# Optimization experiments

Measured on AMD Instinct MI355X. Metric: run time of the kernel, lower is better.

Reference implementation:

```python
import jax, jax.numpy as jnp
import numpy as np

K = 3        # kernel_size
UM = 2       # um_dim
EPS = 1e-6
SLOPE = 0.01 # F.leaky_relu default negative slope


def setup_inputs() -> dict:
    key = jax.random.key(0)
    k1, k2, k3 = jax.random.split(key, 3)
    B, C, H, Wd = 16, 64, 64, 64
    O = 64
    xx = jax.random.normal(k1, (B, C, H, Wd), dtype=jnp.float32)
    W = jax.random.normal(k2, (O, C, K, K), dtype=jnp.float32) * 0.05
    b = jax.random.normal(k3, (O,), dtype=jnp.float32) * 0.05
    return {"xx": xx, "W": W, "b": b}


def reference(xx, W, b):
    B, C, H, Wd = xx.shape
    O = W.shape[0]
    p = (K - 1) // 2
    # replicate pad (mode='replicate' in torch == 'edge' in numpy/jax)
    xp = jnp.pad(xx, ((0, 0), (0, 0), (p, p), (p, p)), mode='edge')
    # unfold -> patches[b, c, i, j, h, w] = xp[b, c, h+i, w+j]; stride==1
    pats = jnp.stack(
        [xp[:, :, i:i + H, j:j + Wd] for i in range(K) for j in range(K)],
        axis=2,
    ).reshape(B, C, K, K, H, Wd)
    # min-max "std" normalization over (channel-group, ki, kj)
    g = pats.reshape(B, C // UM, UM, K, K, H, Wd)
    stds = (g.max(axis=(1, 3, 4), keepdims=True)
            - g.min(axis=(1, 3, 4), keepdims=True))  # [B,1,UM,1,1,H,W]
    normed = (g / (stds + EPS)).reshape(B, C, K, K, H, Wd)
    # patch-conv with stride=k on the unfolded image is equivalent to this
    # per-position contraction; big[b,c,h*k+j, w*k+i] = normed[b,c,i,j,h,w]
    # so the kernel indexes as W[o, c, j, i].
    out = jnp.einsum('bcijhw,ocji->bohw', normed, W) + b[None, :, None, None]
    out = jnp.where(out >= 0, out, SLOPE * out)  # leaky_relu
    # inverse transform: re-scale by (stds + eps)
    stds_s = stds.reshape(B, 1, UM, H, Wd)
    out = out.reshape(B, O // UM, UM, H, Wd) * (stds_s + EPS)
    return out.reshape(B, O, H, Wd)
```

## Files before the change

### kernel.cpp

```cpp
#include <hip/hip_runtime.h>
#include <hip/hip_bf16.h>

#define B_  16
#define C_  64
#define H_  64
#define W_  64
#define O_  64
#define EPS 1e-6f
#define SLOPE 0.01f

typedef __bf16  bf16x8 __attribute__((ext_vector_type(8)));
typedef float   f32x4  __attribute__((ext_vector_type(4)));

#define WLDS_OFF 0
#define WLDS_SZ  92160
#define XT_OFF   92160
#define XT_SZ    36864
#define PMIN_OFF 129024
#define PMAX_OFF 131072
#define SINV_OFF 133120
#define SEPS_OFF 134144
#define SMEM_SZ  135168

__device__ __forceinline__ unsigned short f2bf(float f) {
  unsigned u = __float_as_uint(f);
  u += 0x7fffu + ((u >> 16) & 1u);
  return (unsigned short)(u >> 16);
}

__global__ void wtransform_kernel(const float* __restrict__ Wsrc,
                                  unsigned short* __restrict__ Wt) {
  int idx = blockIdx.x * 256 + threadIdx.x;
  if (idx >= O_ * C_ * 9) return;
  int i = idx % 3;
  int j = (idx / 3) % 3;
  int c = (idx / 9) % C_;
  int o = idx / (9 * C_);
  int tap = i * 3 + j;
  Wt[((tap * 2 + (c & 1)) * 64 + o) * 40 + (c >> 1)] = f2bf(Wsrc[idx]);
}

__device__ __forceinline__ int clampi(int v, int lo, int hi) {
  return v < lo ? lo : (v > hi ? hi : v);
}

__launch_bounds__(256, 1)
__global__ void conv_main_kernel(const float* __restrict__ x,
                                 const unsigned short* __restrict__ Wt,
                                 const float* __restrict__ bias,
                                 float* __restrict__ out) {
  extern __shared__ char smem[];
  const int tid  = threadIdx.x;
  const int lane = tid & 63;
  const int wv   = tid >> 6;
  const int b    = blockIdx.x >> 5;
  const int h0   = (blockIdx.x & 31) << 1;

  {
    const uint4* src = (const uint4*)Wt;
    uint4* dst = (uint4*)(smem + WLDS_OFF);
    for (int k = tid; k < WLDS_SZ / 16; k += 256) dst[k] = src[k];
  }

  {
    const int w = tid & 63;
    const int set = tid >> 6;
    for (int k = 0; k < 8; ++k) {
      const int g = set * 8 + k;
      const int r = g >> 3;
      const int p = (g >> 2) & 1;
      const int m = g & 3;
      const int hr = clampi(h0 - 1 + r, 0, H_ - 1);
      unsigned d[4];
      #pragma unroll
      for (int e = 0; e < 4; ++e) {
        const int c2a = m * 8 + 2 * e;
        const unsigned lo = f2bf(x[((b * C_ + (2 * c2a + p)) * H_ + hr) * W_ + w]);
        const unsigned hi = f2bf(x[((b * C_ + (2 * (c2a + 1) + p)) * H_ + hr) * W_ + w]);
        d[e] = lo | (hi << 16);
      }
      *(uint4*)(smem + XT_OFF + (r * 64 + w) * 144 + p * 64 + m * 16) =
          make_uint4(d[0], d[1], d[2], d[3]);
    }
  }
  __syncthreads();

  {
    const int r = tid >> 6, w = tid & 63;
    const char* rowp = smem + XT_OFF + (r * 64 + w) * 144;
    float* pmin = (float*)(smem + PMIN_OFF);
    float* pmax = (float*)(smem + PMAX_OFF);
    #pragma unroll
    for (int p = 0; p < 2; ++p) {
      float mn = 3.4e38f, mx = -3.4e38f;
      #pragma unroll
      for (int k4 = 0; k4 < 4; ++k4) {
        const uint4 v = *(const uint4*)(rowp + p * 64 + k4 * 16);
        const unsigned dd[4] = {v.x, v.y, v.z, v.w};
        #pragma unroll
        for (int e = 0; e < 4; ++e) {
          const float a = __uint_as_float(dd[e] << 16);
          const float c = __uint_as_float(dd[e] & 0xffff0000u);
          mn = fminf(mn, fminf(a, c));
          mx = fmaxf(mx, fmaxf(a, c));
        }
      }
      pmin[(p * 4 + r) * 64 + w] = mn;
      pmax[(p * 4 + r) * 64 + w] = mx;
    }
  }
  __syncthreads();

  {
    const int hh = tid >> 7, p = (tid >> 6) & 1, w = tid & 63;
    const float* pmin = (const float*)(smem + PMIN_OFF);
    const float* pmax = (const float*)(smem + PMAX_OFF);
    float mn = 3.4e38f, mx = -3.4e38f;
    #pragma unroll
    for (int r = 0; r < 3; ++r) {
      #pragma unroll
      for (int dw = -1; dw <= 1; ++dw) {
        const int wc = clampi(w + dw, 0, W_ - 1);
        mn = fminf(mn, pmin[(p * 4 + (hh + r)) * 64 + wc]);
        mx = fmaxf(mx, pmax[(p * 4 + (hh + r)) * 64 + wc]);
      }
    }
    const float sv = (mx - mn) + EPS;
    ((float*)(smem + SEPS_OFF))[(hh * 2 + p) * 64 + w] = sv;
    ((float*)(smem + SINV_OFF))[(hh * 2 + p) * 64 + w] = 1.0f / sv;
  }
  __syncthreads();

  const int hh  = wv >> 1;
  const int mt2 = wv & 1;
  const int l15 = lane & 15;
  const int q   = lane >> 4;

  const f32x4 zero = {0.0f, 0.0f, 0.0f, 0.0f};
  f32x4 acc[2][2][4];
  #pragma unroll
  for (int p = 0; p < 2; ++p)
    #pragma unroll
    for (int mt = 0; mt < 2; ++mt)
      #pragma unroll
      for (int nt = 0; nt < 4; ++nt) acc[p][mt][nt] = zero;

  for (int tap = 0; tap < 9; ++tap) {
    const int i = tap / 3, j = tap % 3;
    const int xr = hh + i;
    #pragma unroll
    for (int p = 0; p < 2; ++p) {
      bf16x8 af[2], bfr[4];
      #pragma unroll
      for (int mt = 0; mt < 2; ++mt)
        af[mt] = *(const bf16x8*)(smem + WLDS_OFF +
                   ((tap * 2 + p) * 64 + mt2 * 32 + mt * 16 + l15) * 80 + q * 16);
      #pragma unroll
      for (int nt = 0; nt < 4; ++nt) {
        const int wc = clampi(nt * 16 + l15 + j - 1, 0, W_ - 1);
        bfr[nt] = *(const bf16x8*)(smem + XT_OFF + (xr * 64 + wc) * 144 + p * 64 + q * 16);
      }
      #pragma unroll
      for (int mt = 0; mt < 2; ++mt)
        #pragma unroll
        for (int nt = 0; nt < 4; ++nt)
          acc[p][mt][nt] = __builtin_amdgcn_mfma_f32_16x16x32_bf16(
              af[mt], bfr[nt], acc[p][mt][nt], 0, 0, 0);
    }
  }

  const float* sinv = (const float*)(smem + SINV_OFF);
  const float* seps = (const float*)(smem + SEPS_OFF);
  #pragma unroll
  for (int mt = 0; mt < 2; ++mt) {
    #pragma unroll
    for (int reg = 0; reg < 4; ++reg) {
      const int o = mt2 * 32 + mt * 16 + q * 4 + reg;
      const float bv = bias[o];
      #pragma unroll
      for (int nt = 0; nt < 4; ++nt) {
        const int wpx = nt * 16 + l15;
        float v = acc[0][mt][nt][reg] * sinv[(hh * 2 + 0) * 64 + wpx]
                + acc[1][mt][nt][reg] * sinv[(hh * 2 + 1) * 64 + wpx]
                + bv;
        v = v >= 0.0f ? v : SLOPE * v;
        v *= seps[(hh * 2 + (o & 1)) * 64 + wpx];
        out[((b * O_ + o) * H_ + (h0 + hh)) * W_ + wpx] = v;
      }
    }
  }
}

extern "C" void kernel_launch(void* const* d_in, const int* in_sizes, int n_in,
                              void* d_out, int out_size, void* d_ws, size_t ws_size,
                              hipStream_t stream) {
  const float* x    = (const float*)d_in[0];
  const float* Wsrc = (const float*)d_in[1];
  const float* bias = (const float*)d_in[2];
  float* out = (float*)d_out;
  unsigned short* Wt = (unsigned short*)d_ws;

  wtransform_kernel<<<144, 256, 0, stream>>>(Wsrc, Wt);

  (void)hipFuncSetAttribute((const void*)conv_main_kernel,
                            hipFuncAttributeMaxDynamicSharedMemorySize, SMEM_SZ);
  conv_main_kernel<<<512, 256, SMEM_SZ, stream>>>(x, Wt, bias, out);
}
```

Before: 92.28 us.

## Drop weight LDS staging, hold weights in registers, fuse min/max into load

The weights are no longer copied into LDS (about 90KB per block). Each wave now owns 16 output channels and loads its 9 tap A-fragments straight from global memory into registers. Shared memory shrinks to about 43KB, so launch bounds ask for 3 blocks per CU to raise occupancy. The min/max reduction is folded into the fp32 load loop, which removes one LDS pass and a barrier, and each loaded B fragment row is reused across both output rows. The costs are higher register pressure from nine A fragments and the accumulators, and repeated global/L2 reads of the weights by every block.

```diff
diff --git a/kernel.cpp b/kernel.cpp
--- a/kernel.cpp
+++ b/kernel.cpp
@@ -12,20 +12,24 @@
 typedef __bf16  bf16x8 __attribute__((ext_vector_type(8)));
 typedef float   f32x4  __attribute__((ext_vector_type(4)));
 
-#define WLDS_OFF 0
-#define WLDS_SZ  92160
-#define XT_OFF   92160
+#define XT_OFF   0
 #define XT_SZ    36864
-#define PMIN_OFF 129024
-#define PMAX_OFF 131072
-#define SINV_OFF 133120
-#define SEPS_OFF 134144
-#define SMEM_SZ  135168
+#define PMIN_OFF 36864
+#define PMAX_OFF 38912
+#define SINV_OFF 40960
+#define SEPS_OFF 42000
+#undef  SEPS_OFF
+#define SEPS_OFF 41984
+#define SMEM_SZ  43008
 
 __device__ __forceinline__ unsigned short f2bf(float f) {
   unsigned u = __float_as_uint(f);
   u += 0x7fffu + ((u >> 16) & 1u);
   return (unsigned short)(u >> 16);
+}
+
+__device__ __forceinline__ int clampi(int v, int lo, int hi) {
+  return v < lo ? lo : (v > hi ? hi : v);
 }
 
 __global__ void wtransform_kernel(const float* __restrict__ Wsrc,
@@ -37,19 +41,15 @@
   int c = (idx / 9) % C_;
   int o = idx / (9 * C_);
   int tap = i * 3 + j;
-  Wt[((tap * 2 + (c & 1)) * 64 + o) * 40 + (c >> 1)] = f2bf(Wsrc[idx]);
+  Wt[((tap * 2 + (c & 1)) * 64 + o) * 32 + (c >> 1)] = f2bf(Wsrc[idx]);
 }
 
-__device__ __forceinline__ int clampi(int v, int lo, int hi) {
-  return v < lo ? lo : (v > hi ? hi : v);
-}
-
-__launch_bounds__(256, 1)
+__launch_bounds__(256, 3)
 __global__ void conv_main_kernel(const float* __restrict__ x,
                                  const unsigned short* __restrict__ Wt,
                                  const float* __restrict__ bias,
                                  float* __restrict__ out) {
-  extern __shared__ char smem[];
+  __shared__ char smem[SMEM_SZ];
   const int tid  = threadIdx.x;
   const int lane = tid & 63;
   const int wv   = tid >> 6;
@@ -57,57 +57,31 @@
   const int h0   = (blockIdx.x & 31) << 1;
 
   {
-    const uint4* src = (const uint4*)Wt;
-    uint4* dst = (uint4*)(smem + WLDS_OFF);
-    for (int k = tid; k < WLDS_SZ / 16; k += 256) dst[k] = src[k];
-  }
-
-  {
     const int w = tid & 63;
-    const int set = tid >> 6;
-    for (int k = 0; k < 8; ++k) {
-      const int g = set * 8 + k;
-      const int r = g >> 3;
-      const int p = (g >> 2) & 1;
-      const int m = g & 3;
-      const int hr = clampi(h0 - 1 + r, 0, H_ - 1);
+    const int r = tid >> 6;
+    const int hr = clampi(h0 - 1 + r, 0, H_ - 1);
+    const float* xb = x + ((size_t)b * C_ * H_ * W_) + hr * W_ + w;
+    float mn[2] = {3.4e38f, 3.4e38f}, mx[2] = {-3.4e38f, -3.4e38f};
+    #pragma unroll
+    for (int pm = 0; pm < 8; ++pm) {
+      const int p = pm >> 2, m = pm & 3;
       unsigned d[4];
       #pragma unroll
       for (int e = 0; e < 4; ++e) {
         const int c2a = m * 8 + 2 * e;
-        const unsigned lo = f2bf(x[((b * C_ + (2 * c2a + p)) * H_ + hr) * W_ + w]);
-        const unsigned hi = f2bf(x[((b * C_ + (2 * (c2a + 1) + p)) * H_ + hr) * W_ + w]);
-        d[e] = lo | (hi << 16);
+        const float f0 = xb[(2 * c2a + p) * (H_ * W_)];
+        const float f1 = xb[(2 * (c2a + 1) + p) * (H_ * W_)];
+        mn[p] = fminf(mn[p], fminf(f0, f1));
+        mx[p] = fmaxf(mx[p], fmaxf(f0, f1));
+        d[e] = (unsigned)f2bf(f0) | ((unsigned)f2bf(f1) << 16);
       }
       *(uint4*)(smem + XT_OFF + (r * 64 + w) * 144 + p * 64 + m * 16) =
           make_uint4(d[0], d[1], d[2], d[3]);
     }
-  }
-  __syncthreads();
-
-  {
-    const int r = tid >> 6, w = tid & 63;
-    const char* rowp = smem + XT_OFF + (r * 64 + w) * 144;
-    float* pmin = (float*)(smem + PMIN_OFF);
-    float* pmax = (float*)(smem + PMAX_OFF);
-    #pragma unroll
-    for (int p = 0; p < 2; ++p) {
-      float mn = 3.4e38f, mx = -3.4e38f;
-      #pragma unroll
-      for (int k4 = 0; k4 < 4; ++k4) {
-        const uint4 v = *(const uint4*)(rowp + p * 64 + k4 * 16);
-        const unsigned dd[4] = {v.x, v.y, v.z, v.w};
-        #pragma unroll
-        for (int e = 0; e < 4; ++e) {
-          const float a = __uint_as_float(dd[e] << 16);
-          const float c = __uint_as_float(dd[e] & 0xffff0000u);
-          mn = fminf(mn, fminf(a, c));
-          mx = fmaxf(mx, fmaxf(a, c));
-        }
-      }
-      pmin[(p * 4 + r) * 64 + w] = mn;
-      pmax[(p * 4 + r) * 64 + w] = mx;
-    }
+    ((float*)(smem + PMIN_OFF))[(0 * 4 + r) * 64 + w] = mn[0];
+    ((float*)(smem + PMIN_OFF))[(1 * 4 + r) * 64 + w] = mn[1];
+    ((float*)(smem + PMAX_OFF))[(0 * 4 + r) * 64 + w] = mx[0];
+    ((float*)(smem + PMAX_OFF))[(1 * 4 + r) * 64 + w] = mx[1];
   }
   __syncthreads();
 
@@ -131,8 +105,7 @@
   }
   __syncthreads();
 
-  const int hh  = wv >> 1;
-  const int mt2 = wv & 1;
+  const int o0  = wv * 16;
   const int l15 = lane & 15;
   const int q   = lane >> 4;
 
@@ -141,50 +114,57 @@
   #pragma unroll
   for (int p = 0; p < 2; ++p)
     #pragma unroll
-    for (int mt = 0; mt < 2; ++mt)
+    for (int hh = 0; hh < 2; ++hh)
       #pragma unroll
-      for (int nt = 0; nt < 4; ++nt) acc[p][mt][nt] = zero;
+      for (int nt = 0; nt < 4; ++nt) acc[p][hh][nt] = zero;
 
-  for (int tap = 0; tap < 9; ++tap) {
-    const int i = tap / 3, j = tap % 3;
-    const int xr = hh + i;
+  #pragma unroll
+  for (int p = 0; p < 2; ++p) {
+    bf16x8 af[9];
     #pragma unroll
-    for (int p = 0; p < 2; ++p) {
-      bf16x8 af[2], bfr[4];
-      #pragma unroll
-      for (int mt = 0; mt < 2; ++mt)
-        af[mt] = *(const bf16x8*)(smem + WLDS_OFF +
-                   ((tap * 2 + p) * 64 + mt2 * 32 + mt * 16 + l15) * 80 + q * 16);
+    for (int t9 = 0; t9 < 9; ++t9)
+      af[t9] = *(const bf16x8*)(Wt + ((t9 * 2 + p) * 64 + o0 + l15) * 32 + q * 8);
+    #pragma unroll
+    for (int xr = 0; xr < 4; ++xr) {
       #pragma unroll
       for (int nt = 0; nt < 4; ++nt) {
-        const int wc = clampi(nt * 16 + l15 + j - 1, 0, W_ - 1);
-        bfr[nt] = *(const bf16x8*)(smem + XT_OFF + (xr * 64 + wc) * 144 + p * 64 + q * 16);
+        bf16x8 bfr[3];
+        #pragma unroll
+        for (int j = 0; j < 3; ++j) {
+          const int wc = clampi(nt * 16 + l15 + j - 1, 0, W_ - 1);
+          bfr[j] = *(const bf16x8*)(smem + XT_OFF + (xr * 64 + wc) * 144 + p * 64 + q * 16);
+        }
+        #pragma unroll
+        for (int hh = 0; hh < 2; ++hh) {
+          const int i = xr - hh;
+          if (i >= 0 && i < 3) {
+            #pragma unroll
+            for (int j = 0; j < 3; ++j)
+              acc[p][hh][nt] = __builtin_amdgcn_mfma_f32_16x16x32_bf16(
+                  af[i * 3 + j], bfr[j], acc[p][hh][nt], 0, 0, 0);
+          }
+        }
       }
-      #pragma unroll
-      for (int mt = 0; mt < 2; ++mt)
-        #pragma unroll
-        for (int nt = 0; nt < 4; ++nt)
-          acc[p][mt][nt] = __builtin_amdgcn_mfma_f32_16x16x32_bf16(
-              af[mt], bfr[nt], acc[p][mt][nt], 0, 0, 0);
     }
   }
 
   const float* sinv = (const float*)(smem + SINV_OFF);
   const float* seps = (const float*)(smem + SEPS_OFF);
   #pragma unroll
-  for (int mt = 0; mt < 2; ++mt) {
+  for (int hh = 0; hh < 2; ++hh) {
     #pragma unroll
-    for (int reg = 0; reg < 4; ++reg) {
-      const int o = mt2 * 32 + mt * 16 + q * 4 + reg;
-      const float bv = bias[o];
+    for (int nt = 0; nt < 4; ++nt) {
+      const int wpx = nt * 16 + l15;
+      const float s0 = sinv[(hh * 2 + 0) * 64 + wpx];
+      const float s1 = sinv[(hh * 2 + 1) * 64 + wpx];
+      const float se0 = seps[(hh * 2 + 0) * 64 + wpx];
+      const float se1 = seps[(hh * 2 + 1) * 64 + wpx];
       #pragma unroll
-      for (int nt = 0; nt < 4; ++nt) {
-        const int wpx = nt * 16 + l15;
-        float v = acc[0][mt][nt][reg] * sinv[(hh * 2 + 0) * 64 + wpx]
-                + acc[1][mt][nt][reg] * sinv[(hh * 2 + 1) * 64 + wpx]
-                + bv;
+      for (int reg = 0; reg < 4; ++reg) {
+        const int o = o0 + q * 4 + reg;
+        float v = acc[0][hh][nt][reg] * s0 + acc[1][hh][nt][reg] * s1 + bias[o];
         v = v >= 0.0f ? v : SLOPE * v;
-        v *= seps[(hh * 2 + (o & 1)) * 64 + wpx];
+        v *= (o & 1) ? se1 : se0;
         out[((b * O_ + o) * H_ + (h0 + hh)) * W_ + wpx] = v;
       }
     }
@@ -201,8 +181,5 @@
   unsigned short* Wt = (unsigned short*)d_ws;
 
   wtransform_kernel<<<144, 256, 0, stream>>>(Wsrc, Wt);
-
-  (void)hipFuncSetAttribute((const void*)conv_main_kernel,
-                            hipFuncAttributeMaxDynamicSharedMemorySize, SMEM_SZ);
-  conv_main_kernel<<<512, 256, SMEM_SZ, stream>>>(x, Wt, bias, out);
+  conv_main_kernel<<<512, 256, 0, stream>>>(x, Wt, bias, out);
 }
```

After: 82.44 us. 1.12x faster.
